# Kernel tuning notes

Hardware: AMD Instinct MI355X
Metric: run time of the kernel (lower is better)

Reference implementation:

```python
import jax, jax.numpy as jnp
import numpy as np

N = 50000        # n_nodes
E = 640000       # n_edges
D = 128          # d_model (in_dim == out_dim)
H = 8            # num_heads
DH = D // H      # head dim = 16
EPS = 1e-5


def _batchnorm(x, g, b):
    # BatchNorm1d, training-mode batch statistics (biased variance)
    mu = jnp.mean(x, axis=0)
    var = jnp.mean((x - mu) ** 2, axis=0)
    return (x - mu) * jax.lax.rsqrt(var + EPS) * g + b


def setup_inputs() -> dict:
    key = jax.random.key(0)
    ks = jax.random.split(key, 16)
    s = 0.05
    h = jax.random.normal(ks[0], (N, D), jnp.float32)
    src = jax.random.randint(ks[1], (E,), 0, N)
    # guarantee every node has >= 1 incoming edge (avoids z == 0)
    dst = jnp.concatenate([jnp.arange(N), jax.random.randint(ks[2], (E - N,), 0, N)])
    return {
        "h": h,
        "src": src,
        "dst": dst,
        "WQ": jax.random.normal(ks[3], (D, D), jnp.float32) * s,
        "WK": jax.random.normal(ks[4], (D, D), jnp.float32) * s,
        "WV": jax.random.normal(ks[5], (D, D), jnp.float32) * s,
        "WO": jax.random.normal(ks[6], (D, D), jnp.float32) * s,
        "bO": jnp.zeros((D,), jnp.float32),
        "W1": jax.random.normal(ks[7], (2 * D, D), jnp.float32) * s,
        "b1": jnp.zeros((2 * D,), jnp.float32),
        "W2": jax.random.normal(ks[8], (D, 2 * D), jnp.float32) * s,
        "b2": jnp.zeros((D,), jnp.float32),
        "bn1_g": jnp.ones((D,), jnp.float32),
        "bn1_b": jnp.zeros((D,), jnp.float32),
        "bn2_g": jnp.ones((D,), jnp.float32),
        "bn2_b": jnp.zeros((D,), jnp.float32),
    }


def reference(h, src, dst, WQ, WK, WV, WO, bO, W1, b1, W2, b2, bn1_g, bn1_b, bn2_g, bn2_b):
    n = h.shape[0]
    # projections -> [N, H, DH]
    Q = (h @ WQ.T).reshape(n, H, DH)
    K = (h @ WK.T).reshape(n, H, DH)
    V = (h @ WV.T).reshape(n, H, DH)
    # per-edge score: sum(K[src] * Q[dst]) -> [E, H]; clamp/exp (scaled_exp)
    score = jnp.sum(K[src] * Q[dst], axis=-1) / np.sqrt(DH)
    score = jnp.exp(jnp.clip(score, -5.0, 5.0))
    # scatter-sum weighted values and normalizers to destination nodes
    wV = jax.ops.segment_sum(V[src] * score[..., None], dst, num_segments=n)  # [N,H,DH]
    z = jax.ops.segment_sum(score, dst, num_segments=n)                       # [N,H]
    attn = (wV / z[..., None]).reshape(n, D)
    # O projection + residual + BN1
    h1 = _batchnorm(h + (attn @ WO.T + bO), bn1_g, bn1_b)
    # FFN + residual + BN2
    f = jax.nn.relu(h1 @ W1.T + b1) @ W2.T + b2
    return _batchnorm(h1 + f, bn2_g, bn2_b)
```

## Files before the change

kernel.cpp:

```cpp
#include <hip/hip_runtime.h>
#include <math.h>


#define ND128 16384
typedef _Float16 f16;
typedef __attribute__((ext_vector_type(8))) _Float16 h8;
typedef __attribute__((ext_vector_type(4))) _Float16 h4;
typedef __attribute__((ext_vector_type(2))) _Float16 h2;
typedef __attribute__((ext_vector_type(4))) float f4;
typedef __attribute__((ext_vector_type(2))) float ff2;

__device__ __forceinline__ float fast_exp2(float x) {
#if __has_builtin(__builtin_amdgcn_exp2f)
    return __builtin_amdgcn_exp2f(x);
#else
    return exp2f(x);
#endif
}

template <int CTRL>
__device__ __forceinline__ float dppadd(float x) {
    int t = __builtin_amdgcn_update_dpp(0, __float_as_int(x), CTRL, 0xF, 0xF, false);
    return x + __int_as_float(t);
}
__device__ __forceinline__ float wsum8(float p) {
    p = dppadd<0xB1>(p);
    p = dppadd<0x4E>(p);
    p = dppadd<0x141>(p);
    return p;
}

__device__ __forceinline__ ff2 fp8x2_dec_sw(unsigned v) {
    ff2 r;
    unsigned b0 = v & 0xffu, b1 = (v >> 8) & 0xffu;
    {
        unsigned e = (b0 >> 3) & 15u, m = b0 & 7u;
        float x = e ? __uint_as_float(((e + 120u) << 23) | (m << 20)) : (float)m * 0.001953125f;
        r.x = (b0 & 0x80u) ? -x : x;
    }
    {
        unsigned e = (b1 >> 3) & 15u, m = b1 & 7u;
        float x = e ? __uint_as_float(((e + 120u) << 23) | (m << 20)) : (float)m * 0.001953125f;
        r.y = (b1 & 0x80u) ? -x : x;
    }
    return r;
}

__device__ __forceinline__ ff2 dec_lo(unsigned v) {
#if __has_builtin(__builtin_amdgcn_cvt_pk_f32_fp8)
    return __builtin_amdgcn_cvt_pk_f32_fp8((int)v, false);
#else
    return fp8x2_dec_sw(v & 0xffffu);
#endif
}
__device__ __forceinline__ ff2 dec_hi(unsigned v) {
#if __has_builtin(__builtin_amdgcn_cvt_pk_f32_fp8)
    return __builtin_amdgcn_cvt_pk_f32_fp8((int)v, true);
#else
    return fp8x2_dec_sw((v >> 16) & 0xffffu);
#endif
}

#if !__has_builtin(__builtin_amdgcn_cvt_pk_fp8_f32)
__device__ __forceinline__ unsigned char fp8_1(float f) {
    float a = fabsf(f);
    unsigned sg = (__float_as_uint(f) >> 31) << 7;
    if (a >= 448.f) return (unsigned char)(sg | 0x7E);
    if (a < 0.0009765625f) return (unsigned char)sg;
    int E; float m = frexpf(a, &E);
    if (E - 1 < -6) {
        int q = (int)rintf(a * 512.f);
        if (q > 7) return (unsigned char)(sg | 0x08);
        return (unsigned char)(sg | q);
    }
    int q = (int)rintf(m * 16.f);
    if (q == 16) { q = 8; E += 1; }
    int Ef = E - 1 + 7;
    if (Ef > 15) return (unsigned char)(sg | 0x7E);
    return (unsigned char)(sg | (Ef << 3) | (q - 8));
}
#endif

__device__ __forceinline__ unsigned short fp8_pack2(float a0, float a1) {
#if __has_builtin(__builtin_amdgcn_cvt_pk_fp8_f32)
    int pk = __builtin_amdgcn_cvt_pk_fp8_f32(a0, a1, 0, false);
    return (unsigned short)(pk & 0xffff);
#else
    return (unsigned short)((unsigned)fp8_1(a0) | ((unsigned)fp8_1(a1) << 8));
#endif
}

__global__ __launch_bounds__(256) void k_prep_hist(
    const float* __restrict__ h, f16* __restrict__ hb,
    const float* __restrict__ WQ, const float* __restrict__ WK,
    const float* __restrict__ WV, const float* __restrict__ WO,
    const float* __restrict__ W2,
    f16* __restrict__ Wqb, f16* __restrict__ Wkb,
    f16* __restrict__ Wvb, f16* __restrict__ Wob, f16* __restrict__ W2b,
    int* __restrict__ cursor, const int* __restrict__ dst,
    int N, int E, int nhb)
{
    const int tid = threadIdx.x;
    if (blockIdx.x < (unsigned)nhb) {
        int e = blockIdx.x * 256 + tid;
        if (e < E) atomicAdd(&cursor[dst[e]], 1);
        return;
    }
    const int p = blockIdx.x - nhb;
    const int slab = p >> 1, my = p & 1;
#pragma unroll
    for (int it2 = 0; it2 < 4; ++it2) {
        int it = my * 4 + it2;
        int cid = it * 256 + tid;
        int lane = cid & 63;
        int m = (cid >> 6) & 7;
        int kb = cid >> 9;
        int row = slab * 128 + m * 16 + (lane & 15);
        int col = kb * 32 + (lane >> 4) * 8;
        f16 o8[8];
        if (row < N) {
            const float* pp = h + (size_t)row * 128 + col;
            float4 f0 = *(const float4*)pp;
            float4 f1 = *(const float4*)(pp + 4);
            o8[0] = (f16)f0.x; o8[1] = (f16)f0.y; o8[2] = (f16)f0.z; o8[3] = (f16)f0.w;
            o8[4] = (f16)f1.x; o8[5] = (f16)f1.y; o8[6] = (f16)f1.z; o8[7] = (f16)f1.w;
        } else {
#pragma unroll
            for (int j = 0; j < 8; ++j) o8[j] = (f16)0.f;
        }
        *(h8*)(hb + (size_t)slab * ND128 + (size_t)cid * 8) = *(const h8*)o8;
    }
    if (slab < 6 && my == 1) {
        const float* Wsrc; f16* dstw; int K, base;
        if (slab < 4) {
            Wsrc = slab == 0 ? WQ : slab == 1 ? WK : slab == 2 ? WV : WO;
            dstw = slab == 0 ? Wqb : slab == 1 ? Wkb : slab == 2 ? Wvb : Wob;
            K = 128; base = 0;
        } else {
            Wsrc = W2; dstw = W2b; K = 256; base = (slab - 4) * 2048;
        }
#pragma unroll
        for (int it = 0; it < 8; ++it) {
            int cid = base + it * 256 + tid;
            int lane = cid & 63;
            int kb, nt;
            if (K == 128) { kb = (cid >> 6) & 3; nt = cid >> 8; }
            else          { kb = (cid >> 6) & 7; nt = cid >> 9; }
            int row = nt * 16 + (lane & 15);
            int col = kb * 32 + (lane >> 4) * 8;
            const float* pp = Wsrc + (size_t)row * K + col;
            f16 o8[8];
#pragma unroll
            for (int j = 0; j < 8; ++j) o8[j] = (f16)pp[j];
            *(h8*)(dstw + (size_t)cid * 8) = *(const h8*)o8;
        }
    }
}

__global__ __launch_bounds__(256) void k_qkv(
    const f16* __restrict__ hb, const f16* __restrict__ Wqb,
    const f16* __restrict__ Wkb, const f16* __restrict__ Wvb,
    f16* __restrict__ Qb, unsigned char* __restrict__ KV8, int N)
{
    const int slab = blockIdx.x, oidx = blockIdx.y;
    const int w = threadIdx.x >> 6, lane = threadIdx.x & 63;
    const f16* __restrict__ Wb = oidx == 0 ? Wqb : oidx == 1 ? Wkb : Wvb;
    const f16* A = hb + (size_t)slab * ND128;

    h8 bfr[2][4];
#pragma unroll
    for (int nt = 0; nt < 2; ++nt)
#pragma unroll
        for (int kb = 0; kb < 4; ++kb)
            bfr[nt][kb] = *(const h8*)(Wb + (size_t)(((2 * w + nt) * 4 + kb) * 64 + lane) * 8);

    f4 acc[8][2];
    f4 zero = {0.f, 0.f, 0.f, 0.f};
#pragma unroll
    for (int m = 0; m < 8; ++m) { acc[m][0] = zero; acc[m][1] = zero; }

#pragma unroll
    for (int m = 0; m < 8; ++m) {
#pragma unroll
        for (int kb = 0; kb < 4; ++kb) {
            h8 a = *(const h8*)(A + (size_t)((kb * 8 + m) * 64 + lane) * 8);
            acc[m][0] = __builtin_amdgcn_mfma_f32_16x16x32_f16(bfr[0][kb], a, acc[m][0], 0, 0, 0);
            acc[m][1] = __builtin_amdgcn_mfma_f32_16x16x32_f16(bfr[1][kb], a, acc[m][1], 0, 0, 0);
        }
    }

    const int rl = lane & 15, quad = lane >> 4;
    if (oidx == 0) {
#pragma unroll
        for (int m = 0; m < 8; ++m) {
            int gr = slab * 128 + m * 16 + rl;
            if (gr < N) {
#pragma unroll
                for (int nt = 0; nt < 2; ++nt) {
                    h4 o;
                    o[0] = (f16)acc[m][nt][0]; o[1] = (f16)acc[m][nt][1];
                    o[2] = (f16)acc[m][nt][2]; o[3] = (f16)acc[m][nt][3];
                    *(h4*)(Qb + (size_t)gr * 128 + w * 32 + nt * 16 + quad * 4) = o;
                }
            }
        }
    } else {
        const int koff = (oidx == 2) ? 2 : 0;
#pragma unroll
        for (int m = 0; m < 8; ++m) {
            int gr = slab * 128 + m * 16 + rl;
            if (gr < N) {
#pragma unroll
                for (int nt = 0; nt < 2; ++nt) {
                    int c0 = w * 32 + nt * 16 + quad * 4;
                    unsigned short p01 = fp8_pack2(acc[m][nt][0], acc[m][nt][1]);
                    unsigned short p23 = fp8_pack2(acc[m][nt][2], acc[m][nt][3]);
                    unsigned char* rowp = KV8 + (size_t)gr * 256 + (size_t)c0 * 2 + koff;
                    *(unsigned short*)(rowp) = p01;
                    *(unsigned short*)(rowp + 4) = p23;
                }
            }
        }
    }
}

__global__ __launch_bounds__(256) void k_scanA(
    const int* __restrict__ cnt, int* __restrict__ bsum, int N)
{
    const int t = threadIdx.x;
    int base = blockIdx.x * 2048 + t * 8;
    int s = 0;
#pragma unroll
    for (int j = 0; j < 8; ++j) {
        int idx = base + j;
        if (idx < N) s += cnt[idx];
    }
#pragma unroll
    for (int off = 32; off; off >>= 1) s += __shfl_down(s, off, 64);
    __shared__ int ws4[4];
    if ((t & 63) == 0) ws4[t >> 6] = s;
    __syncthreads();
    if (t == 0) bsum[blockIdx.x] = ws4[0] + ws4[1] + ws4[2] + ws4[3];
}

__global__ __launch_bounds__(256) void k_scanC(
    const int* __restrict__ cnt, const int* __restrict__ bsum,
    int* __restrict__ rowptr, int* __restrict__ cursor, int N, int nsb)
{
    const int t = threadIdx.x, b = blockIdx.x;
    __shared__ int sboff;
    if (t == 0) {
        int r = 0;
        for (int i2 = 0; i2 < b; ++i2) r += bsum[i2];
        sboff = r;
    }
    if (t == 64 && b == nsb - 1) {
        int r = 0;
        for (int i2 = 0; i2 < nsb; ++i2) r += bsum[i2];
        rowptr[N] = r;
    }
    int base = b * 2048 + t * 8;
    int loc[8];
    int s = 0;
#pragma unroll
    for (int j = 0; j < 8; ++j) {
        int idx = base + j;
        loc[j] = (idx < N) ? cnt[idx] : 0;
        s += loc[j];
    }
    __shared__ int part[256];
    part[t] = s;
    __syncthreads();
    for (int off = 1; off < 256; off <<= 1) {
        int v = (t >= off) ? part[t - off] : 0;
        __syncthreads();
        part[t] += v;
        __syncthreads();
    }
    int run = sboff + (t ? part[t - 1] : 0);
#pragma unroll
    for (int j = 0; j < 8; ++j) {
        int idx = base + j;
        if (idx < N) { rowptr[idx] = run; cursor[idx] = run; run += loc[j]; }
    }
}

__global__ __launch_bounds__(256) void k_scatter(
    const int* __restrict__ src, const int* __restrict__ dst,
    int* __restrict__ cursor, int* __restrict__ csr_src, int E)
{
    int e = blockIdx.x * 256 + threadIdx.x;
    if (e < E) {
        int pos = atomicAdd(&cursor[dst[e]], 1);
        csr_src[pos] = src[e];
    }
}

__global__ __launch_bounds__(256) void k_attn(
    const f16* __restrict__ Qb, const unsigned char* __restrict__ KV8,
    const int* __restrict__ rowptr, const int* __restrict__ csr_src,
    f16* __restrict__ attnf, int N)
{
    const int node = blockIdx.x * 4 + (threadIdx.x >> 6);
    const int lane = threadIdx.x & 63;
    if (node >= N) return;
    const int beg = rowptr[node], end = rowptr[node + 1];

    float qx, qy;
    {
        h2 q2 = ((const h2*)(Qb + (size_t)node * 128))[lane];
        const float SCL = 0.25f * 1.44269504f;
        qx = (float)q2[0] * SCL;
        qy = (float)q2[1] * SCL;
    }
    const float CLP = 5.f * 1.44269504f;
    const unsigned loff = 4u * (unsigned)lane;

    float axA = 0.f, ayA = 0.f, axB = 0.f, ayB = 0.f, zA = 0.f, zB = 0.f;
    int i = beg;
    for (; i + 7 < end; i += 8) {
        int s[8];
#pragma unroll
        for (int u = 0; u < 8; ++u) s[u] = csr_src[i + u];
        unsigned kv[8];
#pragma unroll
        for (int u = 0; u < 8; ++u)
            kv[u] = *(const unsigned*)(KV8 + (size_t)s[u] * 256 + loff);
        float p[8];
#pragma unroll
        for (int u = 0; u < 8; ++u) {
            ff2 kf = dec_lo(kv[u]);
            p[u] = fmaf(qx, kf.x, qy * kf.y);
        }
#pragma unroll
        for (int u = 0; u < 8; ++u) p[u] = wsum8(p[u]);
        float sc[8];
#pragma unroll
        for (int u = 0; u < 8; ++u)
            sc[u] = fast_exp2(fminf(fmaxf(p[u], -CLP), CLP));
#pragma unroll
        for (int u = 0; u < 8; ++u) {
            ff2 vf = dec_hi(kv[u]);
            if (u & 1) {
                axB = fmaf(vf.x, sc[u], axB); ayB = fmaf(vf.y, sc[u], ayB); zB += sc[u];
            } else {
                axA = fmaf(vf.x, sc[u], axA); ayA = fmaf(vf.y, sc[u], ayA); zA += sc[u];
            }
        }
    }
    if (i + 3 < end) {
        int s[4];
#pragma unroll
        for (int u = 0; u < 4; ++u) s[u] = csr_src[i + u];
        unsigned kv[4];
#pragma unroll
        for (int u = 0; u < 4; ++u)
            kv[u] = *(const unsigned*)(KV8 + (size_t)s[u] * 256 + loff);
#pragma unroll
        for (int u = 0; u < 4; ++u) {
            ff2 kf = dec_lo(kv[u]);
            float p = wsum8(fmaf(qx, kf.x, qy * kf.y));
            float scu = fast_exp2(fminf(fmaxf(p, -CLP), CLP));
            ff2 vf = dec_hi(kv[u]);
            if (u & 1) {
                axB = fmaf(vf.x, scu, axB); ayB = fmaf(vf.y, scu, ayB); zB += scu;
            } else {
                axA = fmaf(vf.x, scu, axA); ayA = fmaf(vf.y, scu, ayA); zA += scu;
            }
        }
        i += 4;
    }
    for (; i < end; ++i) {
        int s0 = csr_src[i];
        unsigned kv = *(const unsigned*)(KV8 + (size_t)s0 * 256 + loff);
        ff2 kf = dec_lo(kv);
        float p0 = wsum8(fmaf(qx, kf.x, qy * kf.y));
        float sc0 = fast_exp2(fminf(fmaxf(p0, -CLP), CLP));
        ff2 vf = dec_hi(kv);
        axA = fmaf(vf.x, sc0, axA); ayA = fmaf(vf.y, sc0, ayA);
        zA += sc0;
    }
    float inv = 1.f / (zA + zB);
    h2 o2;
    o2[0] = (f16)((axA + axB) * inv);
    o2[1] = (f16)((ayA + ayB) * inv);
    int slab = node >> 7, m = (node >> 4) & 7, lr = node & 15;
    int kb = lane >> 4, quad2 = (lane & 15) >> 2, j = (lane & 3) * 2;
    *(h2*)(attnf + (size_t)slab * ND128 +
           (size_t)(((kb * 8 + m) * 64 + lr + 16 * quad2) * 8 + j)) = o2;
}

__global__ __launch_bounds__(256) void k_oproj(
    const f16* __restrict__ attnf, const f16* __restrict__ Wob,
    const f16* __restrict__ hbf, const float* __restrict__ bO,
    f16* __restrict__ t1b, float* __restrict__ bn, int N)
{
    __shared__ float csum[128], csq[128];
    const int tid = threadIdx.x, slab = blockIdx.x;
    const int w = tid >> 6, lane = tid & 63;
    if (tid < 128) { csum[tid] = 0.f; csq[tid] = 0.f; }
    __syncthreads();
    const f16* A = attnf + (size_t)slab * ND128;
    const f16* HB = hbf + (size_t)slab * ND128;

    h8 bfr[2][4];
#pragma unroll
    for (int nt = 0; nt < 2; ++nt)
#pragma unroll
        for (int kb = 0; kb < 4; ++kb)
            bfr[nt][kb] = *(const h8*)(Wob + (size_t)(((2 * w + nt) * 4 + kb) * 64 + lane) * 8);

    f4 acc[8][2];
    f4 zero = {0.f, 0.f, 0.f, 0.f};
#pragma unroll
    for (int m = 0; m < 8; ++m) { acc[m][0] = zero; acc[m][1] = zero; }
#pragma unroll
    for (int m = 0; m < 8; ++m) {
#pragma unroll
        for (int kb = 0; kb < 4; ++kb) {
            h8 a = *(const h8*)(A + (size_t)((kb * 8 + m) * 64 + lane) * 8);
            acc[m][0] = __builtin_amdgcn_mfma_f32_16x16x32_f16(bfr[0][kb], a, acc[m][0], 0, 0, 0);
            acc[m][1] = __builtin_amdgcn_mfma_f32_16x16x32_f16(bfr[1][kb], a, acc[m][1], 0, 0, 0);
        }
    }

    const int rl = lane & 15, quad = lane >> 4;
    float4 bo[2];
#pragma unroll
    for (int nt = 0; nt < 2; ++nt)
        bo[nt] = *(const float4*)(bO + w * 32 + nt * 16 + quad * 4);
    float pcs[2][4], pcq[2][4];
#pragma unroll
    for (int nt = 0; nt < 2; ++nt)
#pragma unroll
        for (int r = 0; r < 4; ++r) { pcs[nt][r] = 0.f; pcq[nt][r] = 0.f; }

#pragma unroll
    for (int m = 0; m < 8; ++m) {
        int gr = slab * 128 + m * 16 + rl;
        if (gr < N) {
#pragma unroll
            for (int nt = 0; nt < 2; ++nt) {
                size_t fidx = (size_t)(((w * 8 + m) * 64 + (nt * 2 + (quad >> 1)) * 16 + rl) * 8 +
                                       (quad & 1) * 4);
                h4 hv4 = *(const h4*)(HB + fidx);
                float v0 = acc[m][nt][0] + (float)hv4[0] + bo[nt].x;
                float v1 = acc[m][nt][1] + (float)hv4[1] + bo[nt].y;
                float v2 = acc[m][nt][2] + (float)hv4[2] + bo[nt].z;
                float v3 = acc[m][nt][3] + (float)hv4[3] + bo[nt].w;
                h4 o; o[0] = (f16)v0; o[1] = (f16)v1; o[2] = (f16)v2; o[3] = (f16)v3;
                *(h4*)(t1b + (size_t)slab * ND128 + fidx) = o;
                pcs[nt][0] += v0; pcq[nt][0] += v0 * v0;
                pcs[nt][1] += v1; pcq[nt][1] += v1 * v1;
                pcs[nt][2] += v2; pcq[nt][2] += v2 * v2;
                pcs[nt][3] += v3; pcq[nt][3] += v3 * v3;
            }
        }
    }
#pragma unroll
    for (int nt = 0; nt < 2; ++nt)
#pragma unroll
        for (int r = 0; r < 4; ++r) {
            float s = pcs[nt][r], q = pcq[nt][r];
            s += __shfl_xor(s, 8, 16); q += __shfl_xor(q, 8, 16);
            s += __shfl_xor(s, 4, 16); q += __shfl_xor(q, 4, 16);
            s += __shfl_xor(s, 2, 16); q += __shfl_xor(q, 2, 16);
            s += __shfl_xor(s, 1, 16); q += __shfl_xor(q, 1, 16);
            if (rl == 0) {
                int cl = w * 32 + nt * 16 + quad * 4 + r;
                atomicAdd(&csum[cl], s);
                atomicAdd(&csq[cl], q);
            }
        }
    __syncthreads();
    if (tid < 128) {
        atomicAdd(bn + tid, csum[tid]);
        atomicAdd(bn + 128 + tid, csq[tid]);
    }
}

__global__ __launch_bounds__(128) void k_fold1(
    const float* __restrict__ bn, const float* __restrict__ g1,
    const float* __restrict__ bb1, const float* __restrict__ W1,
    const float* __restrict__ b1, f16* __restrict__ W1b,
    float* __restrict__ badj, float* __restrict__ sfold,
    float* __restrict__ bfold, int N)
{
    const int o = blockIdx.x, i = threadIdx.x;
    float invN = 1.f / (float)N;
    float mu = bn[i] * invN;
    float var = bn[128 + i] * invN - mu * mu;
    float s = g1[i] * rsqrtf(var + 1e-5f);
    float bb = bb1[i] - mu * s;
    if (o == 0) { sfold[i] = s; bfold[i] = bb; }
    float wv = W1[(size_t)o * 128 + i];
    __shared__ float red[128];
    red[i] = wv * bb;
    const int nt = o >> 4, lanelow = o & 15;
    const int kb = i >> 5, quad = (i >> 3) & 3, j = i & 7;
    W1b[(size_t)(((nt * 4 + kb) * 64 + lanelow + 16 * quad) * 8 + j)] = (f16)(wv * s);
    __syncthreads();
#pragma unroll
    for (int off = 64; off; off >>= 1) {
        if (i < off) red[i] += red[i + off];
        __syncthreads();
    }
    if (i == 0) badj[o] = b1[o] + red[0];
}

__global__ __launch_bounds__(256) void k_ffn1(
    const f16* __restrict__ t1b, const f16* __restrict__ W1b,
    const float* __restrict__ badj, f16* __restrict__ ub, int N)
{
    const int slab = blockIdx.x, ch = blockIdx.y;
    const int w = threadIdx.x >> 6, lane = threadIdx.x & 63;
    const f16* A = t1b + (size_t)slab * ND128;

    h8 bfr[2][4];
#pragma unroll
    for (int nt = 0; nt < 2; ++nt)
#pragma unroll
        for (int kb = 0; kb < 4; ++kb) {
            int ntg = ch * 8 + 2 * w + nt;
            bfr[nt][kb] = *(const h8*)(W1b + (size_t)((ntg * 4 + kb) * 64 + lane) * 8);
        }

    f4 acc[8][2];
    f4 zero = {0.f, 0.f, 0.f, 0.f};
#pragma unroll
    for (int m = 0; m < 8; ++m) { acc[m][0] = zero; acc[m][1] = zero; }
#pragma unroll
    for (int m = 0; m < 8; ++m) {
#pragma unroll
        for (int kb = 0; kb < 4; ++kb) {
            h8 a = *(const h8*)(A + (size_t)((kb * 8 + m) * 64 + lane) * 8);
            acc[m][0] = __builtin_amdgcn_mfma_f32_16x16x32_f16(bfr[0][kb], a, acc[m][0], 0, 0, 0);
            acc[m][1] = __builtin_amdgcn_mfma_f32_16x16x32_f16(bfr[1][kb], a, acc[m][1], 0, 0, 0);
        }
    }

    const int rl = lane & 15, quad = lane >> 4;
    const int kbu = ch * 4 + w;
    float4 ba[2];
#pragma unroll
    for (int nt = 0; nt < 2; ++nt)
        ba[nt] = *(const float4*)(badj + ch * 128 + w * 32 + nt * 16 + quad * 4);
#pragma unroll
    for (int m = 0; m < 8; ++m) {
        int gr = slab * 128 + m * 16 + rl;
        if (gr < N) {
#pragma unroll
            for (int nt = 0; nt < 2; ++nt) {
                h4 o;
                o[0] = (f16)fmaxf(acc[m][nt][0] + ba[nt].x, 0.f);
                o[1] = (f16)fmaxf(acc[m][nt][1] + ba[nt].y, 0.f);
                o[2] = (f16)fmaxf(acc[m][nt][2] + ba[nt].z, 0.f);
                o[3] = (f16)fmaxf(acc[m][nt][3] + ba[nt].w, 0.f);
                *(h4*)(ub + (size_t)slab * 32768 +
                       (size_t)(((kbu * 8 + m) * 64 + (nt * 2 + (quad >> 1)) * 16 + rl) * 8 +
                                (quad & 1) * 4)) = o;
            }
        }
    }
}

__global__ __launch_bounds__(256) void k_ffn2(
    const f16* __restrict__ ub, const f16* __restrict__ W2b,
    const f16* __restrict__ t1b,
    const float* __restrict__ sfold, const float* __restrict__ bfold,
    const float* __restrict__ b2, f16* __restrict__ t2f,
    float* __restrict__ bn, int N)
{
    __shared__ float csum[128], csq[128], sS[128], sB[128];
    const int tid = threadIdx.x, slab = blockIdx.x;
    const int w = tid >> 6, lane = tid & 63;
    if (tid < 128) {
        csum[tid] = 0.f; csq[tid] = 0.f;
        sS[tid] = sfold[tid]; sB[tid] = bfold[tid] + b2[tid];
    }
    __syncthreads();
    const f16* A = ub + (size_t)slab * 32768;
    const f16* T1 = t1b + (size_t)slab * ND128;

    h8 bfr[2][8];
#pragma unroll
    for (int nt = 0; nt < 2; ++nt)
#pragma unroll
        for (int kb = 0; kb < 8; ++kb)
            bfr[nt][kb] = *(const h8*)(W2b + (size_t)(((2 * w + nt) * 8 + kb) * 64 + lane) * 8);

    f4 acc[8][2];
    f4 zero = {0.f, 0.f, 0.f, 0.f};
#pragma unroll
    for (int m = 0; m < 8; ++m) { acc[m][0] = zero; acc[m][1] = zero; }
#pragma unroll
    for (int m = 0; m < 8; ++m) {
#pragma unroll
        for (int kb = 0; kb < 8; ++kb) {
            h8 a = *(const h8*)(A + (size_t)((kb * 8 + m) * 64 + lane) * 8);
            acc[m][0] = __builtin_amdgcn_mfma_f32_16x16x32_f16(bfr[0][kb], a, acc[m][0], 0, 0, 0);
            acc[m][1] = __builtin_amdgcn_mfma_f32_16x16x32_f16(bfr[1][kb], a, acc[m][1], 0, 0, 0);
        }
    }

    const int rl = lane & 15, quad = lane >> 4;
    float pcs[2][4], pcq[2][4];
#pragma unroll
    for (int nt = 0; nt < 2; ++nt)
#pragma unroll
        for (int r = 0; r < 4; ++r) { pcs[nt][r] = 0.f; pcq[nt][r] = 0.f; }

#pragma unroll
    for (int m = 0; m < 8; ++m) {
        int gr = slab * 128 + m * 16 + rl;
        if (gr < N) {
#pragma unroll
            for (int nt = 0; nt < 2; ++nt) {
                int col0 = w * 32 + nt * 16 + quad * 4;
                size_t fidx = (size_t)(((w * 8 + m) * 64 + (nt * 2 + (quad >> 1)) * 16 + rl) * 8 +
                                       (quad & 1) * 4);
                h4 t1v = *(const h4*)(T1 + fidx);
                float4 ss = *(const float4*)&sS[col0];
                float4 sb = *(const float4*)&sB[col0];
                h4 o2;
                o2[0] = (f16)(acc[m][nt][0] + fmaf(ss.x, (float)t1v[0], sb.x));
                o2[1] = (f16)(acc[m][nt][1] + fmaf(ss.y, (float)t1v[1], sb.y));
                o2[2] = (f16)(acc[m][nt][2] + fmaf(ss.z, (float)t1v[2], sb.z));
                o2[3] = (f16)(acc[m][nt][3] + fmaf(ss.w, (float)t1v[3], sb.w));
                *(h4*)(t2f + (size_t)slab * ND128 + fidx) = o2;
                float r0 = (float)o2[0], r1 = (float)o2[1];
                float r2 = (float)o2[2], r3 = (float)o2[3];
                pcs[nt][0] += r0; pcq[nt][0] += r0 * r0;
                pcs[nt][1] += r1; pcq[nt][1] += r1 * r1;
                pcs[nt][2] += r2; pcq[nt][2] += r2 * r2;
                pcs[nt][3] += r3; pcq[nt][3] += r3 * r3;
            }
        }
    }
#pragma unroll
    for (int nt = 0; nt < 2; ++nt)
#pragma unroll
        for (int r = 0; r < 4; ++r) {
            float s = pcs[nt][r], q = pcq[nt][r];
            s += __shfl_xor(s, 8, 16); q += __shfl_xor(q, 8, 16);
            s += __shfl_xor(s, 4, 16); q += __shfl_xor(q, 4, 16);
            s += __shfl_xor(s, 2, 16); q += __shfl_xor(q, 2, 16);
            s += __shfl_xor(s, 1, 16); q += __shfl_xor(q, 1, 16);
            if (rl == 0) {
                int cl = w * 32 + nt * 16 + quad * 4 + r;
                atomicAdd(&csum[cl], s);
                atomicAdd(&csq[cl], q);
            }
        }
    __syncthreads();
    if (tid < 128) {
        atomicAdd(bn + 256 + tid, csum[tid]);
        atomicAdd(bn + 384 + tid, csq[tid]);
    }
}

__global__ __launch_bounds__(256) void k_bn2(
    const f16* __restrict__ t2f, float* __restrict__ out,
    const float* __restrict__ bn,
    const float* __restrict__ g2, const float* __restrict__ bb2, int N)
{
    __shared__ float sS[128], sB[128];
    const int tid = threadIdx.x;
    if (tid < 128) {
        float invN = 1.f / (float)N;
        float mu = bn[256 + tid] * invN;
        float var = bn[384 + tid] * invN - mu * mu;
        float scl = g2[tid] * rsqrtf(var + 1e-5f);
        sS[tid] = scl;
        sB[tid] = bb2[tid] - mu * scl;
    }
    __syncthreads();
    size_t idx = (size_t)blockIdx.x * 256 + tid;
    size_t total = (size_t)N * 32;
    if (idx < total) {
        int gr = (int)(idx >> 5);
        int c0 = ((int)idx & 31) * 4;
        int slab = gr >> 7, m = (gr >> 4) & 7, rl = gr & 15;
        int w = c0 >> 5, nt = (c0 >> 4) & 1, q = (c0 >> 2) & 3;
        size_t fidx = (size_t)(((w * 8 + m) * 64 + (nt * 2 + (q >> 1)) * 16 + rl) * 8 +
                               (q & 1) * 4);
        h4 v = *(const h4*)(t2f + (size_t)slab * ND128 + fidx);
        float4 o;
        o.x = fmaf((float)v[0], sS[c0 + 0], sB[c0 + 0]);
        o.y = fmaf((float)v[1], sS[c0 + 1], sB[c0 + 1]);
        o.z = fmaf((float)v[2], sS[c0 + 2], sB[c0 + 2]);
        o.w = fmaf((float)v[3], sS[c0 + 3], sB[c0 + 3]);
        *(float4*)(out + (size_t)gr * 128 + c0) = o;
    }
}

extern "C" void kernel_launch(void* const* d_in, const int* in_sizes, int n_in,
                              void* d_out, int out_size, void* d_ws, size_t ws_size,
                              hipStream_t stream)
{
    const float* h   = (const float*)d_in[0];
    const int*   src = (const int*)d_in[1];
    const int*   dst = (const int*)d_in[2];
    const float* WQ  = (const float*)d_in[3];
    const float* WK  = (const float*)d_in[4];
    const float* WV  = (const float*)d_in[5];
    const float* WO  = (const float*)d_in[6];
    const float* bO  = (const float*)d_in[7];
    const float* W1  = (const float*)d_in[8];
    const float* b1  = (const float*)d_in[9];
    const float* W2  = (const float*)d_in[10];
    const float* b2  = (const float*)d_in[11];
    const float* g1  = (const float*)d_in[12];
    const float* bb1 = (const float*)d_in[13];
    const float* g2  = (const float*)d_in[14];
    const float* bb2 = (const float*)d_in[15];
    float* out = (float*)d_out;

    int N = in_sizes[0] / 128;
    int E = in_sizes[1];
    int slabs = (N + 127) / 128;
    int nsb = (N + 2047) / 2048;
    int nhb = (E + 255) / 256;
    const size_t B1 = (size_t)slabs * 32768;

    char* Wp = (char*)d_ws;
    f16* hb  = (f16*)Wp;
    f16* Qb  = (f16*)(Wp + B1);
    unsigned char* KV8 = (unsigned char*)(Wp + 2 * B1);
    f16* attnf = (f16*)(Wp + 3 * B1);
    f16* t1b = (f16*)(Wp + 4 * B1);
    f16* ub  = (f16*)(Wp + B1);
    f16* t2f = attnf;
    const size_t base = 5 * B1;
    f16* Wqb = (f16*)(Wp + base);
    f16* Wkb = (f16*)(Wp + base + 32768);
    f16* Wvb = (f16*)(Wp + base + 65536);
    f16* Wob = (f16*)(Wp + base + 98304);
    f16* W1b = (f16*)(Wp + base + 131072);
    f16* W2b = (f16*)(Wp + base + 196608);
    float* badj  = (float*)(Wp + base + 262144);
    float* sfold = (float*)(Wp + base + 263168);
    float* bfold = (float*)(Wp + base + 263680);
    float* bn    = (float*)(Wp + base + 264192);
    int* bsum    = (int*)(Wp + base + 266240);
    int* cursor  = (int*)(Wp + base + 266496);
    int* rowptr  = (int*)(Wp + base + 266496 + (size_t)N * 4);
    int* csr     = (int*)(Wp + base + 266496 + (size_t)N * 8 + 8);

    hipMemsetAsync(Wp + base + 264192, 0, 2304 + (size_t)N * 4, stream);
    k_prep_hist<<<nhb + slabs * 2, 256, 0, stream>>>(
        h, hb, WQ, WK, WV, WO, W2, Wqb, Wkb, Wvb, Wob, W2b, cursor, dst, N, E, nhb);
    k_qkv<<<dim3(slabs, 3), 256, 0, stream>>>(hb, Wqb, Wkb, Wvb, Qb, KV8, N);
    k_scanA<<<nsb, 256, 0, stream>>>(cursor, bsum, N);
    k_scanC<<<nsb, 256, 0, stream>>>(cursor, bsum, rowptr, cursor, N, nsb);
    k_scatter<<<nhb, 256, 0, stream>>>(src, dst, cursor, csr, E);
    k_attn<<<(N + 3) / 4, 256, 0, stream>>>(Qb, KV8, rowptr, csr, attnf, N);
    k_oproj<<<slabs, 256, 0, stream>>>(attnf, Wob, hb, bO, t1b, bn, N);
    k_fold1<<<256, 128, 0, stream>>>(bn, g1, bb1, W1, b1, W1b, badj, sfold, bfold, N);
    k_ffn1<<<dim3(slabs, 2), 256, 0, stream>>>(t1b, W1b, badj, ub, N);
    k_ffn2<<<slabs, 256, 0, stream>>>(ub, W2b, t1b, sfold, bfold, b2, t2f, bn, N);
    k_bn2<<<(int)(((size_t)N * 32 + 255) / 256), 256, 0, stream>>>(t2f, out, bn, g2, bb2, N);
}
```

Before: 310.4 us.

## Fuse h conversion, QKV projection and scan block-sum into one kernel

The h-to-fp16 conversion moves out of the prep/histogram kernel into a new 512-thread QKV kernel. That kernel stages each 128-row slab in shared memory and computes Q, K and V from it in sequence, replacing the three separate blocks per slab that each re-read hb from global memory. The scanA block-sum work is folded into extra blocks of the same launch, removing one kernel launch. The cost is 32KB of LDS per block, which lowers occupancy, and less parallelism for the QKV GEMMs, since one block now does three outputs.

```diff
diff --git a/kernel.cpp b/kernel.cpp
--- a/kernel.cpp
+++ b/kernel.cpp
@@ -91,7 +91,6 @@
 }
 
 __global__ __launch_bounds__(256) void k_prep_hist(
-    const float* __restrict__ h, f16* __restrict__ hb,
     const float* __restrict__ WQ, const float* __restrict__ WK,
     const float* __restrict__ WV, const float* __restrict__ WO,
     const float* __restrict__ W2,
@@ -106,12 +105,66 @@
         if (e < E) atomicAdd(&cursor[dst[e]], 1);
         return;
     }
-    const int p = blockIdx.x - nhb;
-    const int slab = p >> 1, my = p & 1;
-#pragma unroll
-    for (int it2 = 0; it2 < 4; ++it2) {
-        int it = my * 4 + it2;
-        int cid = it * 256 + tid;
+    const int ws = blockIdx.x - nhb;
+    const float* Wsrc; f16* dstw; int K, base;
+    if (ws < 4) {
+        Wsrc = ws == 0 ? WQ : ws == 1 ? WK : ws == 2 ? WV : WO;
+        dstw = ws == 0 ? Wqb : ws == 1 ? Wkb : ws == 2 ? Wvb : Wob;
+        K = 128; base = 0;
+    } else {
+        Wsrc = W2; dstw = W2b; K = 256; base = (ws - 4) * 2048;
+    }
+#pragma unroll
+    for (int it = 0; it < 8; ++it) {
+        int cid = base + it * 256 + tid;
+        int lane = cid & 63;
+        int kb, nt;
+        if (K == 128) { kb = (cid >> 6) & 3; nt = cid >> 8; }
+        else          { kb = (cid >> 6) & 7; nt = cid >> 9; }
+        int row = nt * 16 + (lane & 15);
+        int col = kb * 32 + (lane >> 4) * 8;
+        const float* pp = Wsrc + (size_t)row * K + col;
+        f16 o8[8];
+#pragma unroll
+        for (int j = 0; j < 8; ++j) o8[j] = (f16)pp[j];
+        *(h8*)(dstw + (size_t)cid * 8) = *(const h8*)o8;
+    }
+}
+
+__global__ __launch_bounds__(512) void k_qkvf(
+    const float* __restrict__ h, f16* __restrict__ hb,
+    const f16* __restrict__ Wqb, const f16* __restrict__ Wkb,
+    const f16* __restrict__ Wvb,
+    f16* __restrict__ Qb, unsigned char* __restrict__ KV8,
+    const int* __restrict__ cursor, int* __restrict__ bsum, int N, int nsb)
+{
+    __shared__ f16 sA[ND128];
+    __shared__ int ws8[8];
+    const int tid = threadIdx.x;
+    if (blockIdx.x < (unsigned)nsb) {
+        int base = blockIdx.x * 2048 + tid * 4;
+        int s = 0;
+#pragma unroll
+        for (int j = 0; j < 4; ++j) {
+            int idx = base + j;
+            if (idx < N) s += cursor[idx];
+        }
+#pragma unroll
+        for (int off = 32; off; off >>= 1) s += __shfl_down(s, off, 64);
+        if ((tid & 63) == 0) ws8[tid >> 6] = s;
+        __syncthreads();
+        if (tid == 0) {
+            int r = 0;
+#pragma unroll
+            for (int k = 0; k < 8; ++k) r += ws8[k];
+            bsum[blockIdx.x] = r;
+        }
+        return;
+    }
+    const int slab = blockIdx.x - nsb;
+#pragma unroll
+    for (int it = 0; it < 4; ++it) {
+        int cid = it * 512 + tid;
         int lane = cid & 63;
         int m = (cid >> 6) & 7;
         int kb = cid >> 9;
@@ -128,93 +181,54 @@
 #pragma unroll
             for (int j = 0; j < 8; ++j) o8[j] = (f16)0.f;
         }
-        *(h8*)(hb + (size_t)slab * ND128 + (size_t)cid * 8) = *(const h8*)o8;
-    }
-    if (slab < 6 && my == 1) {
-        const float* Wsrc; f16* dstw; int K, base;
-        if (slab < 4) {
-            Wsrc = slab == 0 ? WQ : slab == 1 ? WK : slab == 2 ? WV : WO;
-            dstw = slab == 0 ? Wqb : slab == 1 ? Wkb : slab == 2 ? Wvb : Wob;
-            K = 128; base = 0;
+        h8 v = *(const h8*)o8;
+        *(h8*)(hb + (size_t)slab * ND128 + (size_t)cid * 8) = v;
+        *(h8*)(sA + (size_t)cid * 8) = v;
+    }
+    __syncthreads();
+
+    const int w2 = tid >> 6, lane = tid & 63;
+    const int rl = lane & 15, quad = lane >> 4;
+#pragma unroll
+    for (int oidx = 0; oidx < 3; ++oidx) {
+        const f16* __restrict__ Wb = oidx == 0 ? Wqb : oidx == 1 ? Wkb : Wvb;
+        h8 bfr[4];
+#pragma unroll
+        for (int kb = 0; kb < 4; ++kb)
+            bfr[kb] = *(const h8*)(Wb + (size_t)((w2 * 4 + kb) * 64 + lane) * 8);
+
+        f4 acc[8];
+        f4 zero = {0.f, 0.f, 0.f, 0.f};
+#pragma unroll
+        for (int m = 0; m < 8; ++m) acc[m] = zero;
+#pragma unroll
+        for (int m = 0; m < 8; ++m) {
+#pragma unroll
+            for (int kb = 0; kb < 4; ++kb) {
+                h8 a = *(const h8*)(sA + (size_t)((kb * 8 + m) * 64 + lane) * 8);
+                acc[m] = __builtin_amdgcn_mfma_f32_16x16x32_f16(bfr[kb], a, acc[m], 0, 0, 0);
+            }
+        }
+        if (oidx == 0) {
+#pragma unroll
+            for (int m = 0; m < 8; ++m) {
+                int gr = slab * 128 + m * 16 + rl;
+                if (gr < N) {
+                    h4 o;
+                    o[0] = (f16)acc[m][0]; o[1] = (f16)acc[m][1];
+                    o[2] = (f16)acc[m][2]; o[3] = (f16)acc[m][3];
+                    *(h4*)(Qb + (size_t)gr * 128 + w2 * 16 + quad * 4) = o;
+                }
+            }
         } else {
-            Wsrc = W2; dstw = W2b; K = 256; base = (slab - 4) * 2048;
-        }
-#pragma unroll
-        for (int it = 0; it < 8; ++it) {
-            int cid = base + it * 256 + tid;
-            int lane = cid & 63;
-            int kb, nt;
-            if (K == 128) { kb = (cid >> 6) & 3; nt = cid >> 8; }
-            else          { kb = (cid >> 6) & 7; nt = cid >> 9; }
-            int row = nt * 16 + (lane & 15);
-            int col = kb * 32 + (lane >> 4) * 8;
-            const float* pp = Wsrc + (size_t)row * K + col;
-            f16 o8[8];
-#pragma unroll
-            for (int j = 0; j < 8; ++j) o8[j] = (f16)pp[j];
-            *(h8*)(dstw + (size_t)cid * 8) = *(const h8*)o8;
-        }
-    }
-}
-
-__global__ __launch_bounds__(256) void k_qkv(
-    const f16* __restrict__ hb, const f16* __restrict__ Wqb,
-    const f16* __restrict__ Wkb, const f16* __restrict__ Wvb,
-    f16* __restrict__ Qb, unsigned char* __restrict__ KV8, int N)
-{
-    const int slab = blockIdx.x, oidx = blockIdx.y;
-    const int w = threadIdx.x >> 6, lane = threadIdx.x & 63;
-    const f16* __restrict__ Wb = oidx == 0 ? Wqb : oidx == 1 ? Wkb : Wvb;
-    const f16* A = hb + (size_t)slab * ND128;
-
-    h8 bfr[2][4];
-#pragma unroll
-    for (int nt = 0; nt < 2; ++nt)
-#pragma unroll
-        for (int kb = 0; kb < 4; ++kb)
-            bfr[nt][kb] = *(const h8*)(Wb + (size_t)(((2 * w + nt) * 4 + kb) * 64 + lane) * 8);
-
-    f4 acc[8][2];
-    f4 zero = {0.f, 0.f, 0.f, 0.f};
-#pragma unroll
-    for (int m = 0; m < 8; ++m) { acc[m][0] = zero; acc[m][1] = zero; }
-
-#pragma unroll
-    for (int m = 0; m < 8; ++m) {
-#pragma unroll
-        for (int kb = 0; kb < 4; ++kb) {
-            h8 a = *(const h8*)(A + (size_t)((kb * 8 + m) * 64 + lane) * 8);
-            acc[m][0] = __builtin_amdgcn_mfma_f32_16x16x32_f16(bfr[0][kb], a, acc[m][0], 0, 0, 0);
-            acc[m][1] = __builtin_amdgcn_mfma_f32_16x16x32_f16(bfr[1][kb], a, acc[m][1], 0, 0, 0);
-        }
-    }
-
-    const int rl = lane & 15, quad = lane >> 4;
-    if (oidx == 0) {
-#pragma unroll
-        for (int m = 0; m < 8; ++m) {
-            int gr = slab * 128 + m * 16 + rl;
-            if (gr < N) {
-#pragma unroll
-                for (int nt = 0; nt < 2; ++nt) {
-                    h4 o;
-                    o[0] = (f16)acc[m][nt][0]; o[1] = (f16)acc[m][nt][1];
-                    o[2] = (f16)acc[m][nt][2]; o[3] = (f16)acc[m][nt][3];
-                    *(h4*)(Qb + (size_t)gr * 128 + w * 32 + nt * 16 + quad * 4) = o;
-                }
-            }
-        }
-    } else {
-        const int koff = (oidx == 2) ? 2 : 0;
-#pragma unroll
-        for (int m = 0; m < 8; ++m) {
-            int gr = slab * 128 + m * 16 + rl;
-            if (gr < N) {
-#pragma unroll
-                for (int nt = 0; nt < 2; ++nt) {
-                    int c0 = w * 32 + nt * 16 + quad * 4;
-                    unsigned short p01 = fp8_pack2(acc[m][nt][0], acc[m][nt][1]);
-                    unsigned short p23 = fp8_pack2(acc[m][nt][2], acc[m][nt][3]);
+            const int koff = (oidx == 2) ? 2 : 0;
+#pragma unroll
+            for (int m = 0; m < 8; ++m) {
+                int gr = slab * 128 + m * 16 + rl;
+                if (gr < N) {
+                    int c0 = w2 * 16 + quad * 4;
+                    unsigned short p01 = fp8_pack2(acc[m][0], acc[m][1]);
+                    unsigned short p23 = fp8_pack2(acc[m][2], acc[m][3]);
                     unsigned char* rowp = KV8 + (size_t)gr * 256 + (size_t)c0 * 2 + koff;
                     *(unsigned short*)(rowp) = p01;
                     *(unsigned short*)(rowp + 4) = p23;
@@ -222,25 +236,6 @@
             }
         }
     }
-}
-
-__global__ __launch_bounds__(256) void k_scanA(
-    const int* __restrict__ cnt, int* __restrict__ bsum, int N)
-{
-    const int t = threadIdx.x;
-    int base = blockIdx.x * 2048 + t * 8;
-    int s = 0;
-#pragma unroll
-    for (int j = 0; j < 8; ++j) {
-        int idx = base + j;
-        if (idx < N) s += cnt[idx];
-    }
-#pragma unroll
-    for (int off = 32; off; off >>= 1) s += __shfl_down(s, off, 64);
-    __shared__ int ws4[4];
-    if ((t & 63) == 0) ws4[t >> 6] = s;
-    __syncthreads();
-    if (t == 0) bsum[blockIdx.x] = ws4[0] + ws4[1] + ws4[2] + ws4[3];
 }
 
 __global__ __launch_bounds__(256) void k_scanC(
@@ -748,10 +743,10 @@
     int* csr     = (int*)(Wp + base + 266496 + (size_t)N * 8 + 8);
 
     hipMemsetAsync(Wp + base + 264192, 0, 2304 + (size_t)N * 4, stream);
-    k_prep_hist<<<nhb + slabs * 2, 256, 0, stream>>>(
-        h, hb, WQ, WK, WV, WO, W2, Wqb, Wkb, Wvb, Wob, W2b, cursor, dst, N, E, nhb);
-    k_qkv<<<dim3(slabs, 3), 256, 0, stream>>>(hb, Wqb, Wkb, Wvb, Qb, KV8, N);
-    k_scanA<<<nsb, 256, 0, stream>>>(cursor, bsum, N);
+    k_prep_hist<<<nhb + 6, 256, 0, stream>>>(
+        WQ, WK, WV, WO, W2, Wqb, Wkb, Wvb, Wob, W2b, cursor, dst, N, E, nhb);
+    k_qkvf<<<nsb + slabs, 512, 0, stream>>>(
+        h, hb, Wqb, Wkb, Wvb, Qb, KV8, cursor, bsum, N, nsb);
     k_scanC<<<nsb, 256, 0, stream>>>(cursor, bsum, rowptr, cursor, N, nsb);
     k_scatter<<<nhb, 256, 0, stream>>>(src, dst, cursor, csr, E);
     k_attn<<<(N + 3) / 4, 256, 0, stream>>>(Qb, KV8, rowptr, csr, attnf, N);
```

New measurement: 298.2 us. -3.9%, faster.
